# Kernel tuning notes

Measured on AMD Instinct MI355X. Metric: run time of the kernel, lower is better.

## Reference

```python
import jax, jax.numpy as jnp
import numpy as np
from jax import lax

T, B, E = 4096, 8, 512


def setup_inputs() -> dict:
    key = jax.random.key(0)
    k1, k2, k3 = jax.random.split(key, 3)
    x = jax.random.normal(k1, (T, B, E), dtype=jnp.float32)
    raw_pos_beta = jax.random.normal(k2, (E,), dtype=jnp.float32)
    raw_neg_beta = jax.random.normal(k3, (E,), dtype=jnp.float32)
    return {"x": x, "raw_pos_beta": raw_pos_beta, "raw_neg_beta": raw_neg_beta}


def reference(x, raw_pos_beta, raw_neg_beta):
    # pos/neg split EMA. The torch module computes out[t] = sum_{s<=t} beta^(t-s) u[s]
    # via a length-T depthwise conv; that is exactly the linear recurrence
    # mem[t] = beta * mem[t-1] + u[t], which we run as an O(T) scan.
    pos_beta = jax.nn.sigmoid(raw_pos_beta)  # [E]
    neg_beta = jax.nn.sigmoid(raw_neg_beta)  # [E]
    x_pos = jnp.where(x >= 0, x, 0.0) * (1.0 - pos_beta)  # [T,B,E]
    x_neg = jnp.where(x <= 0, x, 0.0) * (1.0 - neg_beta)  # [T,B,E]
    u = jnp.stack([x_pos, x_neg], axis=-1)                # [T,B,E,2]
    beta = jnp.stack([pos_beta, neg_beta], axis=-1)       # [E,2]

    def step(carry, u_t):
        new = beta * carry + u_t  # [B,E,2]
        return new, new

    init = jnp.zeros(u.shape[1:], dtype=x.dtype)
    _, mem2 = lax.scan(step, init, u)  # [T,B,E,2]
    return mem2[..., 0] + mem2[..., 1]  # [T,B,E]
```

## Files before the change

kernel.cpp:

```cpp
#include <hip/hip_runtime.h>


#define T_DIM 4096
#define B_DIM 8
#define E_DIM 512
#define CHUNK_L 16
#define NCHUNK (T_DIM / CHUNK_L)
#define BE (B_DIM * E_DIM)

__device__ __forceinline__ float sigmoidf_(float x) { return 1.0f / (1.0f + __expf(-x)); }

__global__ __launch_bounds__(256) void ParallelDLIEMA_17789754541002_kernel(
        const float* __restrict__ x,
        const float* __restrict__ rp,
        const float* __restrict__ rn,
        float* __restrict__ out) {
    int gtid = blockIdx.x * 256 + threadIdx.x;
    int e4 = gtid & 127;
    int b  = (gtid >> 7) & 7;
    int c  = gtid >> 10;
    int e  = e4 * 4;

    float4 rp4 = *(const float4*)(rp + e);
    float4 rn4 = *(const float4*)(rn + e);
    float bp[4] = {sigmoidf_(rp4.x), sigmoidf_(rp4.y), sigmoidf_(rp4.z), sigmoidf_(rp4.w)};
    float bn[4] = {sigmoidf_(rn4.x), sigmoidf_(rn4.y), sigmoidf_(rn4.z), sigmoidf_(rn4.w)};

    float fp4[4] = {0.f, 0.f, 0.f, 0.f};
    float fn4[4] = {0.f, 0.f, 0.f, 0.f};
    int base = c * CHUNK_L * BE + b * E_DIM + e;
    #pragma unroll
    for (int k = 0; k < CHUNK_L; k++) {
        float4 xv = *(const float4*)(x + base + k * BE);
        float f[4] = {xv.x, xv.y, xv.z, xv.w};
        #pragma unroll
        for (int j = 0; j < 4; j++) {
            fp4[j] = bp[j] * fp4[j] + fmaxf(f[j], 0.f) * (1.0f - bp[j]);
            fn4[j] = bn[j] * fn4[j] + fminf(f[j], 0.f) * (1.0f - bn[j]);
        }
    }
    *(float4*)(out + base + 0 * BE) = make_float4(fp4[0], fp4[1], fp4[2], fp4[3]);
    *(float4*)(out + base + 1 * BE) = make_float4(fn4[0], fn4[1], fn4[2], fn4[3]);
}

__global__ __launch_bounds__(256) void k_carry(const float* __restrict__ rp,
                                               const float* __restrict__ rn,
                                               float* __restrict__ out) {
    int gtid = blockIdx.x * 256 + threadIdx.x;
    int e = gtid & 511;
    int b = (gtid >> 9) & 7;
    int s = gtid >> 12;
    float beta = sigmoidf_(s ? rn[e] : rp[e]);
    float bl = beta * beta; bl = bl * bl; bl = bl * bl; bl = bl * bl;

    float* p = out + s * BE + b * E_DIM + e;
    float carry = 0.f;
    for (int g = 0; g < NCHUNK / 16; g++) {
        float fv[16];
        #pragma unroll
        for (int u = 0; u < 16; u++) fv[u] = p[(g * 16 + u) * (CHUNK_L * BE)];
        #pragma unroll
        for (int u = 0; u < 16; u++) {
            p[(g * 16 + u) * (CHUNK_L * BE)] = carry;
            carry = bl * carry + fv[u];
        }
    }
}

__global__ __launch_bounds__(256) void k_out(const float* __restrict__ x,
                                             const float* __restrict__ rp,
                                             const float* __restrict__ rn,
                                             float* __restrict__ out) {
    int gtid = blockIdx.x * 256 + threadIdx.x;
    int e4 = gtid & 127;
    int b  = (gtid >> 7) & 7;
    int c  = gtid >> 10;
    int e  = e4 * 4;

    float4 rp4 = *(const float4*)(rp + e);
    float4 rn4 = *(const float4*)(rn + e);
    float bp[4] = {sigmoidf_(rp4.x), sigmoidf_(rp4.y), sigmoidf_(rp4.z), sigmoidf_(rp4.w)};
    float bn[4] = {sigmoidf_(rn4.x), sigmoidf_(rn4.y), sigmoidf_(rn4.z), sigmoidf_(rn4.w)};

    int base = c * CHUNK_L * BE + b * E_DIM + e;
    float4 cp = *(const float4*)(out + base + 0 * BE);
    float4 cn = *(const float4*)(out + base + 1 * BE);
    float lp[4] = {cp.x, cp.y, cp.z, cp.w};
    float ln[4] = {cn.x, cn.y, cn.z, cn.w};

    #pragma unroll
    for (int k = 0; k < CHUNK_L; k++) {
        float4 xv = *(const float4*)(x + base + k * BE);
        float f[4] = {xv.x, xv.y, xv.z, xv.w};
        float o[4];
        #pragma unroll
        for (int j = 0; j < 4; j++) {
            lp[j] = bp[j] * lp[j] + fmaxf(f[j], 0.f) * (1.0f - bp[j]);
            ln[j] = bn[j] * ln[j] + fminf(f[j], 0.f) * (1.0f - bn[j]);
            o[j] = lp[j] + ln[j];
        }
        *(float4*)(out + base + k * BE) = make_float4(o[0], o[1], o[2], o[3]);
    }
}

extern "C" void kernel_launch(void* const* d_in, const int* in_sizes, int n_in,
                              void* d_out, int out_size, void* d_ws, size_t ws_size,
                              hipStream_t stream) {
    const float* x  = (const float*)d_in[0];
    const float* rp = (const float*)d_in[1];
    const float* rn = (const float*)d_in[2];
    float* out = (float*)d_out;

    ParallelDLIEMA_17789754541002_kernel<<<1024, 256, 0, stream>>>(x, rp, rn, out);
    k_carry<<<32, 256, 0, stream>>>(rp, rn, out);
    k_out<<<1024, 256, 0, stream>>>(x, rp, rn, out);
}
```

Measured before the change: 135.9 us.

## Replace serial carry kernel with per-chunk prefix over workspace aggregates

When a large enough workspace is available, the three-kernel scheme becomes two kernels. The first writes each chunk's pos/neg local aggregates (chunk length 32) into the workspace. The second has each thread scan all preceding chunk aggregates to rebuild its incoming carry, then recomputes its chunk and writes the output. This removes the low-parallelism 32-block carry kernel and one launch. The cost is a quadratic number of aggregate reads (up to 127 chunks per thread, mostly cache hits), and the old path is kept as a fallback.

```diff
diff --git a/kernel.cpp b/kernel.cpp
--- a/kernel.cpp
+++ b/kernel.cpp
@@ -4,33 +4,116 @@
 #define T_DIM 4096
 #define B_DIM 8
 #define E_DIM 512
-#define CHUNK_L 16
+#define CHUNK_L 32
 #define NCHUNK (T_DIM / CHUNK_L)
 #define BE (B_DIM * E_DIM)
 
 __device__ __forceinline__ float sigmoidf_(float x) { return 1.0f / (1.0f + __expf(-x)); }
 
-__global__ __launch_bounds__(256) void ParallelDLIEMA_17789754541002_kernel(
+__global__ __launch_bounds__(256) void k_agg(
         const float* __restrict__ x,
         const float* __restrict__ rp,
         const float* __restrict__ rn,
-        float* __restrict__ out) {
-    int gtid = blockIdx.x * 256 + threadIdx.x;
-    int e4 = gtid & 127;
-    int b  = (gtid >> 7) & 7;
-    int c  = gtid >> 10;
-    int e  = e4 * 4;
+        float* __restrict__ agg) {
+    const int gtid = blockIdx.x * 256 + threadIdx.x;
+    const int q = gtid & 1023;
+    const int c = gtid >> 10;
+    const int e = (q & 127) * 4;
+    const int b = q >> 7;
+    const int col = b * E_DIM + e;
 
     float4 rp4 = *(const float4*)(rp + e);
     float4 rn4 = *(const float4*)(rn + e);
     float bp[4] = {sigmoidf_(rp4.x), sigmoidf_(rp4.y), sigmoidf_(rp4.z), sigmoidf_(rp4.w)};
     float bn[4] = {sigmoidf_(rn4.x), sigmoidf_(rn4.y), sigmoidf_(rn4.z), sigmoidf_(rn4.w)};
 
-    float fp4[4] = {0.f, 0.f, 0.f, 0.f};
-    float fn4[4] = {0.f, 0.f, 0.f, 0.f};
-    int base = c * CHUNK_L * BE + b * E_DIM + e;
+    float fp[4] = {0.f, 0.f, 0.f, 0.f};
+    float fn[4] = {0.f, 0.f, 0.f, 0.f};
+    const int xbase = c * CHUNK_L * BE + col;
     #pragma unroll
     for (int k = 0; k < CHUNK_L; k++) {
+        float4 xv = *(const float4*)(x + xbase + k * BE);
+        float f[4] = {xv.x, xv.y, xv.z, xv.w};
+        #pragma unroll
+        for (int j = 0; j < 4; j++) {
+            fp[j] = bp[j] * fp[j] + fmaxf(f[j], 0.f) * (1.0f - bp[j]);
+            fn[j] = bn[j] * fn[j] + fminf(f[j], 0.f) * (1.0f - bn[j]);
+        }
+    }
+    *(float4*)(agg + (size_t)(c * 2 + 0) * BE + col) = make_float4(fp[0], fp[1], fp[2], fp[3]);
+    *(float4*)(agg + (size_t)(c * 2 + 1) * BE + col) = make_float4(fn[0], fn[1], fn[2], fn[3]);
+}
+
+__global__ __launch_bounds__(256) void ParallelDLIEMA_17789754541002_kernel(
+        const float* __restrict__ x,
+        const float* __restrict__ rp,
+        const float* __restrict__ rn,
+        const float* __restrict__ agg,
+        float* __restrict__ out) {
+    const int gtid = blockIdx.x * 256 + threadIdx.x;
+    const int q = gtid & 1023;
+    const int c = gtid >> 10;
+    const int e = (q & 127) * 4;
+    const int b = q >> 7;
+    const int col = b * E_DIM + e;
+
+    float4 rp4 = *(const float4*)(rp + e);
+    float4 rn4 = *(const float4*)(rn + e);
+    float bp[4] = {sigmoidf_(rp4.x), sigmoidf_(rp4.y), sigmoidf_(rp4.z), sigmoidf_(rp4.w)};
+    float bn[4] = {sigmoidf_(rn4.x), sigmoidf_(rn4.y), sigmoidf_(rn4.z), sigmoidf_(rn4.w)};
+
+    float Ap[4], An[4];
+    #pragma unroll
+    for (int j = 0; j < 4; j++) {
+        float t = bp[j] * bp[j]; t *= t; t *= t; t *= t; t *= t; Ap[j] = t;
+        float u = bn[j] * bn[j]; u *= u; u *= u; u *= u; u *= u; An[j] = u;
+    }
+
+    float sp[4] = {0.f, 0.f, 0.f, 0.f};
+    float sn[4] = {0.f, 0.f, 0.f, 0.f};
+    #pragma unroll 4
+    for (int j = 0; j < c; ++j) {
+        float4 ap = *(const float4*)(agg + (size_t)(j * 2 + 0) * BE + col);
+        float4 an = *(const float4*)(agg + (size_t)(j * 2 + 1) * BE + col);
+        sp[0] = Ap[0] * sp[0] + ap.x;  sn[0] = An[0] * sn[0] + an.x;
+        sp[1] = Ap[1] * sp[1] + ap.y;  sn[1] = An[1] * sn[1] + an.y;
+        sp[2] = Ap[2] * sp[2] + ap.z;  sn[2] = An[2] * sn[2] + an.z;
+        sp[3] = Ap[3] * sp[3] + ap.w;  sn[3] = An[3] * sn[3] + an.w;
+    }
+
+    const int xbase = c * CHUNK_L * BE + col;
+    #pragma unroll
+    for (int k = 0; k < CHUNK_L; k++) {
+        float4 xv = *(const float4*)(x + xbase + k * BE);
+        float f[4] = {xv.x, xv.y, xv.z, xv.w};
+        float o[4];
+        #pragma unroll
+        for (int j = 0; j < 4; j++) {
+            sp[j] = bp[j] * sp[j] + fmaxf(f[j], 0.f) * (1.0f - bp[j]);
+            sn[j] = bn[j] * sn[j] + fminf(f[j], 0.f) * (1.0f - bn[j]);
+            o[j] = sp[j] + sn[j];
+        }
+        *(float4*)(out + xbase + k * BE) = make_float4(o[0], o[1], o[2], o[3]);
+    }
+}
+
+
+#define FB_CHUNK_L 16
+#define FB_NCHUNK (T_DIM / FB_CHUNK_L)
+
+__global__ __launch_bounds__(256) void k1_local(
+        const float* __restrict__ x, const float* __restrict__ rp,
+        const float* __restrict__ rn, float* __restrict__ out) {
+    int gtid = blockIdx.x * 256 + threadIdx.x;
+    int e4 = gtid & 127; int b = (gtid >> 7) & 7; int c = gtid >> 10; int e = e4 * 4;
+    float4 rp4 = *(const float4*)(rp + e);
+    float4 rn4 = *(const float4*)(rn + e);
+    float bp[4] = {sigmoidf_(rp4.x), sigmoidf_(rp4.y), sigmoidf_(rp4.z), sigmoidf_(rp4.w)};
+    float bn[4] = {sigmoidf_(rn4.x), sigmoidf_(rn4.y), sigmoidf_(rn4.z), sigmoidf_(rn4.w)};
+    float fp4[4] = {0.f,0.f,0.f,0.f}, fn4[4] = {0.f,0.f,0.f,0.f};
+    int base = c * FB_CHUNK_L * BE + b * E_DIM + e;
+    #pragma unroll
+    for (int k = 0; k < FB_CHUNK_L; k++) {
         float4 xv = *(const float4*)(x + base + k * BE);
         float f[4] = {xv.x, xv.y, xv.z, xv.w};
         #pragma unroll
@@ -47,21 +130,18 @@
                                                const float* __restrict__ rn,
                                                float* __restrict__ out) {
     int gtid = blockIdx.x * 256 + threadIdx.x;
-    int e = gtid & 511;
-    int b = (gtid >> 9) & 7;
-    int s = gtid >> 12;
+    int e = gtid & 511; int b = (gtid >> 9) & 7; int s = gtid >> 12;
     float beta = sigmoidf_(s ? rn[e] : rp[e]);
     float bl = beta * beta; bl = bl * bl; bl = bl * bl; bl = bl * bl;
-
     float* p = out + s * BE + b * E_DIM + e;
     float carry = 0.f;
-    for (int g = 0; g < NCHUNK / 16; g++) {
+    for (int g = 0; g < FB_NCHUNK / 16; g++) {
         float fv[16];
         #pragma unroll
-        for (int u = 0; u < 16; u++) fv[u] = p[(g * 16 + u) * (CHUNK_L * BE)];
+        for (int u = 0; u < 16; u++) fv[u] = p[(g * 16 + u) * (FB_CHUNK_L * BE)];
         #pragma unroll
         for (int u = 0; u < 16; u++) {
-            p[(g * 16 + u) * (CHUNK_L * BE)] = carry;
+            p[(g * 16 + u) * (FB_CHUNK_L * BE)] = carry;
             carry = bl * carry + fv[u];
         }
     }
@@ -72,24 +152,18 @@
                                              const float* __restrict__ rn,
                                              float* __restrict__ out) {
     int gtid = blockIdx.x * 256 + threadIdx.x;
-    int e4 = gtid & 127;
-    int b  = (gtid >> 7) & 7;
-    int c  = gtid >> 10;
-    int e  = e4 * 4;
-
+    int e4 = gtid & 127; int b = (gtid >> 7) & 7; int c = gtid >> 10; int e = e4 * 4;
     float4 rp4 = *(const float4*)(rp + e);
     float4 rn4 = *(const float4*)(rn + e);
     float bp[4] = {sigmoidf_(rp4.x), sigmoidf_(rp4.y), sigmoidf_(rp4.z), sigmoidf_(rp4.w)};
     float bn[4] = {sigmoidf_(rn4.x), sigmoidf_(rn4.y), sigmoidf_(rn4.z), sigmoidf_(rn4.w)};
-
-    int base = c * CHUNK_L * BE + b * E_DIM + e;
+    int base = c * FB_CHUNK_L * BE + b * E_DIM + e;
     float4 cp = *(const float4*)(out + base + 0 * BE);
     float4 cn = *(const float4*)(out + base + 1 * BE);
     float lp[4] = {cp.x, cp.y, cp.z, cp.w};
     float ln[4] = {cn.x, cn.y, cn.z, cn.w};
-
     #pragma unroll
-    for (int k = 0; k < CHUNK_L; k++) {
+    for (int k = 0; k < FB_CHUNK_L; k++) {
         float4 xv = *(const float4*)(x + base + k * BE);
         float f[4] = {xv.x, xv.y, xv.z, xv.w};
         float o[4];
@@ -111,7 +185,14 @@
     const float* rn = (const float*)d_in[2];
     float* out = (float*)d_out;
 
-    ParallelDLIEMA_17789754541002_kernel<<<1024, 256, 0, stream>>>(x, rp, rn, out);
-    k_carry<<<32, 256, 0, stream>>>(rp, rn, out);
-    k_out<<<1024, 256, 0, stream>>>(x, rp, rn, out);
+    const size_t need = (size_t)2 * NCHUNK * BE * sizeof(float);
+    if (d_ws != nullptr && ws_size >= need) {
+        float* agg = (float*)d_ws;
+        k_agg<<<512, 256, 0, stream>>>(x, rp, rn, agg);
+        ParallelDLIEMA_17789754541002_kernel<<<512, 256, 0, stream>>>(x, rp, rn, agg, out);
+    } else {
+        k1_local<<<1024, 256, 0, stream>>>(x, rp, rn, out);
+        k_carry<<<32, 256, 0, stream>>>(rp, rn, out);
+        k_out<<<1024, 256, 0, stream>>>(x, rp, rn, out);
+    }
 }
```

Result: faster. 129.7 us (-4.6%).
